# Performance work log

Measured on AMD Instinct MI355X. Metric: run time of the kernel, lower is better.

The kernel has to match this reference:

```python
import jax, jax.numpy as jnp
import numpy as np

NEG_INF = -1e16


def setup_inputs() -> dict:
    key = jax.random.key(0)
    k1, k2, k3 = jax.random.split(key, 3)
    B, N, C, D = 8, 4096, 64, 64
    inputs = jax.random.normal(k1, (B, N, C), dtype=jnp.float32)
    graph = jax.random.randint(k2, (N, N), 0, 2, dtype=jnp.int32)
    # xavier_uniform for Linear weight [D, C]
    limit = float(np.sqrt(6.0 / (C + D)))
    W = jax.random.uniform(k3, (D, C), dtype=jnp.float32, minval=-limit, maxval=limit)
    b = jnp.zeros((D,), dtype=jnp.float32)
    return {"inputs": inputs, "graph": graph, "W": W, "b": b}


def reference(inputs, graph, W, b):
    # h = W(inputs): [B, N, D]
    h = jnp.einsum('bnc,dc->bnd', inputs, W)
    # dense pairwise scores: [B, N, N]
    scores = jnp.einsum('bnd,bmd->bnm', h, h)
    # mask non-edges (graph broadcasts over batch)
    scores = jnp.where(graph[None, :, :] == 0, NEG_INF, scores)
    attention = jax.nn.softmax(scores, axis=2)
    out = jnp.einsum('bnm,bmd->bnd', attention, h) + b
    return out
```

## Files before the change

### kernel.cpp

```cpp
#include <hip/hip_runtime.h>
#include <stdint.h>

typedef _Float16 f16x8 __attribute__((ext_vector_type(8)));
typedef _Float16 f16x4 __attribute__((ext_vector_type(4)));
typedef __fp16 half2_t __attribute__((ext_vector_type(2)));
typedef float f32x4 __attribute__((ext_vector_type(4)));

#define LOG2E 1.44269504088896340736f
#define NEGINF (-1e16f)

constexpr int kN = 4096;
constexpr int kD = 64;
constexpr int kB = 8;

__global__ __launch_bounds__(256) void hproj_kernel(const float* __restrict__ x,
                                                    const float* __restrict__ W,
                                                    _Float16* __restrict__ hout,
                                                    _Float16* __restrict__ hTout)
{
    __shared__ float Wt[64][64];
    __shared__ float xs[64][65];
    __shared__ _Float16 ht[64][68];

    const int tid = threadIdx.x;
    const int r   = tid >> 2;
    const int c0  = (tid & 3) * 16;

    #pragma unroll
    for (int j = 0; j < 16; j += 4) {
        const float4 v = *(const float4*)(W + r * 64 + c0 + j);
        Wt[c0 + j + 0][r] = v.x;
        Wt[c0 + j + 1][r] = v.y;
        Wt[c0 + j + 2][r] = v.z;
        Wt[c0 + j + 3][r] = v.w;
    }
    const long rowbase = (long)blockIdx.x * 64;
    #pragma unroll
    for (int j = 0; j < 16; j += 4) {
        const float4 v = *(const float4*)(x + (rowbase + r) * 64 + c0 + j);
        xs[r][c0 + j + 0] = v.x;
        xs[r][c0 + j + 1] = v.y;
        xs[r][c0 + j + 2] = v.z;
        xs[r][c0 + j + 3] = v.w;
    }
    __syncthreads();

    const int d0 = (tid & 3) * 16;
    f32x4 acc[4] = {{0.f,0.f,0.f,0.f},{0.f,0.f,0.f,0.f},{0.f,0.f,0.f,0.f},{0.f,0.f,0.f,0.f}};
    #pragma unroll 4
    for (int c = 0; c < 64; ++c) {
        const float xv = xs[r][c];
        const f32x4* wrow = (const f32x4*)&Wt[c][d0];
        #pragma unroll
        for (int k = 0; k < 4; ++k) acc[k] += wrow[k] * xv;
    }
    f16x8 o0, o1;
    #pragma unroll
    for (int j = 0; j < 8; ++j) {
        o0[j] = (_Float16)acc[j >> 2][j & 3];
        o1[j] = (_Float16)acc[2 + (j >> 2)][j & 3];
    }
    *(f16x8*)(hout + (rowbase + r) * 64 + d0)     = o0;
    *(f16x8*)(hout + (rowbase + r) * 64 + d0 + 8) = o1;

    #pragma unroll
    for (int j = 0; j < 8; ++j) {
        ht[r][d0 + j]     = o0[j];
        ht[r][d0 + 8 + j] = o1[j];
    }
    __syncthreads();

    const int bb = blockIdx.x >> 6;
    const int n0 = (int)(rowbase & (kN - 1));
    const int dr = tid >> 2;
    const int c4 = (tid & 3) * 16;
    f16x8 t0, t1;
    #pragma unroll
    for (int j = 0; j < 8; ++j) {
        t0[j] = ht[c4 + j][dr];
        t1[j] = ht[c4 + 8 + j][dr];
    }
    _Float16* dst = hTout + (long)bb * kD * kN + (long)dr * kN + n0 + c4;
    *(f16x8*)(dst)     = t0;
    *(f16x8*)(dst + 8) = t1;
}

__global__ __launch_bounds__(256) void bitpack_kernel(const int* __restrict__ g,
                                                      uint32_t* __restrict__ mw)
{
    const long w = (long)blockIdx.x * 256 + threadIdx.x;
    const int4* p = (const int4*)(g + w * 32);
    uint32_t bits = 0;
    #pragma unroll
    for (int j = 0; j < 8; ++j) {
        const int4 v = p[j];
        bits |= (uint32_t)(v.x != 0) << (j * 4 + 0);
        bits |= (uint32_t)(v.y != 0) << (j * 4 + 1);
        bits |= (uint32_t)(v.z != 0) << (j * 4 + 2);
        bits |= (uint32_t)(v.w != 0) << (j * 4 + 3);
    }
    mw[w] = bits;
}

__global__ __launch_bounds__(256) void masktr_kernel(const uint32_t* __restrict__ mw,
                                                     uint64_t* __restrict__ wmout)
{
    const int tid  = threadIdx.x;
    const int wv   = tid >> 6;
    const int lane = tid & 63;
    const int ll   = lane & 15;
    const int lg   = lane >> 4;
    const int pair = blockIdx.x * 4 + wv;
    const int q16  = pair >> 6;
    const int kv64 = pair & 63;

    const uint2 u = *(const uint2*)(mw + (long)(q16 * 16 + ll) * 128 + kv64 * 2);

    uint64_t Wb[16];
    #pragma unroll
    for (int s = 0; s < 16; ++s) {
        const int t = s >> 2, rr = s & 3;
        const uint32_t word = (t >= 2) ? u.y : u.x;
        const int pos = 8 * lg + 4 * (t & 1) + rr;
        Wb[s] = __ballot(((word >> pos) & 1u) != 0);
    }

    const int s = lane;
    uint64_t a0 = (s & 1) ? Wb[1]  : Wb[0];
    uint64_t a1 = (s & 1) ? Wb[3]  : Wb[2];
    uint64_t a2 = (s & 1) ? Wb[5]  : Wb[4];
    uint64_t a3 = (s & 1) ? Wb[7]  : Wb[6];
    uint64_t a4 = (s & 1) ? Wb[9]  : Wb[8];
    uint64_t a5 = (s & 1) ? Wb[11] : Wb[10];
    uint64_t a6 = (s & 1) ? Wb[13] : Wb[12];
    uint64_t a7 = (s & 1) ? Wb[15] : Wb[14];
    uint64_t b0 = (s & 2) ? a1 : a0;
    uint64_t b1 = (s & 2) ? a3 : a2;
    uint64_t b2 = (s & 2) ? a5 : a4;
    uint64_t b3 = (s & 2) ? a7 : a6;
    uint64_t c0 = (s & 4) ? b1 : b0;
    uint64_t c1 = (s & 4) ? b3 : b2;
    uint64_t v  = (s & 8) ? c1 : c0;
    if (lane < 16) wmout[(long)pair * 16 + lane] = v;
}

__global__ __launch_bounds__(512, 4) void attn_kernel(const _Float16* __restrict__ h,
                                                      const _Float16* __restrict__ hT,
                                                      const uint64_t* __restrict__ wmask,
                                                      const float* __restrict__ bias,
                                                      float* __restrict__ outp,
                                                      _Float16* __restrict__ pO,
                                                      float* __restrict__ pml,
                                                      int kvlen)
{
    __shared__ alignas(16) char Kl[2][8192];
    __shared__ alignas(16) char Vt[2][8192];

    const int b     = blockIdx.y;
    const int split = blockIdx.z;
    const int q0    = blockIdx.x * 256;
    const int tid   = threadIdx.x;
    const int wave  = tid >> 6;
    const int lane  = tid & 63;
    const int lg    = lane >> 4;
    const int ll    = lane & 15;

    const _Float16* hb  = h  + (long)b * kN * kD;
    const _Float16* hTb = hT + (long)b * kD * kN;
    const int kv_base = split * kvlen;
    const int NT      = kvlen / 64;

    const int qA = q0 + wave * 32 + ll;
    const int qB = qA + 16;
    const f16x8 qfA0 = *(const f16x8*)(hb + qA * 64 + lg * 8);
    const f16x8 qfA1 = *(const f16x8*)(hb + qA * 64 + 32 + lg * 8);
    const f16x8 qfB0 = *(const f16x8*)(hb + qB * 64 + lg * 8);
    const f16x8 qfB1 = *(const f16x8*)(hb + qB * 64 + 32 + lg * 8);

    f16x8 vone;
    {
        const _Float16 o = (ll == 0) ? (_Float16)1.0f : (_Float16)0.0f;
        #pragma unroll
        for (int j = 0; j < 8; ++j) vone[j] = o;
    }

    f32x4 OaccA[4] = {{0.f,0.f,0.f,0.f},{0.f,0.f,0.f,0.f},{0.f,0.f,0.f,0.f},{0.f,0.f,0.f,0.f}};
    f32x4 OaccB[4] = {{0.f,0.f,0.f,0.f},{0.f,0.f,0.f,0.f},{0.f,0.f,0.f,0.f},{0.f,0.f,0.f,0.f}};
    f32x4 Oacc4A = {0.f, 0.f, 0.f, 0.f};
    f32x4 Oacc4B = {0.f, 0.f, 0.f, 0.f};
    float m_runA = NEGINF, m_runB = NEGINF;
    float mmA = NEGINF * LOG2E, mmB = NEGINF * LOG2E;
    float negv = NEGINF;

    const int sr  = tid >> 3;
    const int sc8 = (tid & 7) * 8;
    const int srp = (sr & 0x23) | ((sr & 0x18) >> 1) | ((sr & 0x4) << 2);

    const int kw = srp * 128 + ((sc8 * 2) ^ ((srp & 7) << 4));
    const int vw = sr  * 128 + ((sc8 * 2) ^ ((sr  & 7) << 4));
    const int rb0 = ll * 128 + (((lg * 16))      ^ ((ll & 7) << 4));
    const int rb1 = ll * 128 + (((64 + lg * 16)) ^ ((ll & 7) << 4));

    char* const KB = (char*)Kl;
    char* const VB = (char*)Vt;

    const _Float16* gK = hb  + (long)(kv_base + sr) * 64 + sc8;
    const _Float16* gV = hTb + (long)sr * kN + kv_base + sc8;

    const int wuni = __builtin_amdgcn_readfirstlane(wave);
    const uint64_t* __restrict__ wmpA =
        wmask + ((long)(blockIdx.x * 16 + wuni * 2) * 64 + (kv_base >> 6)) * 16;
    const uint64_t* __restrict__ wmpB = wmpA + (long)64 * 16;

    {
        const f16x8 a0 = *(const f16x8*)(gK);
        const f16x8 b0 = *(const f16x8*)(gV);
        *(f16x8*)(KB + kw) = a0;
        *(f16x8*)(VB + vw) = b0;
        gK += 64 * 64;  gV += 64;
    }

    union PF { half2_t hh[4]; f16x8 v; };

#define SOFTMAX_FRAG(S_, WM_, OACC_, OACC4_, MRUN_, MM_, PF1_, PF2_)             \
    do {                                                                         \
        _Pragma("unroll")                                                        \
        for (int t = 0; t < 4; ++t) {                                            \
            _Pragma("unroll")                                                    \
            for (int rr = 0; rr < 4; ++rr) {                                     \
                float sv = S_[t][rr];                                            \
                asm("v_cndmask_b32 %0, %1, %2, %3"                               \
                    : "=v"(sv) : "v"(negv), "v"(sv), "s"(WM_[t * 4 + rr]));      \
                S_[t][rr] = sv;                                                  \
            }                                                                    \
        }                                                                        \
        float mx0 = fmaxf(fmaxf(S_[0][0], S_[0][1]), fmaxf(S_[0][2], S_[0][3])); \
        float mx1 = fmaxf(fmaxf(S_[1][0], S_[1][1]), fmaxf(S_[1][2], S_[1][3])); \
        float mx2 = fmaxf(fmaxf(S_[2][0], S_[2][1]), fmaxf(S_[2][2], S_[2][3])); \
        float mx3 = fmaxf(fmaxf(S_[3][0], S_[3][1]), fmaxf(S_[3][2], S_[3][3])); \
        float mloc = fmaxf(fmaxf(mx0, mx1), fmaxf(mx2, mx3));                    \
        mloc = fmaxf(mloc, __shfl_xor(mloc, 16));                                \
        mloc = fmaxf(mloc, __shfl_xor(mloc, 32));                                \
        if (__any(mloc > MRUN_ + 8.f)) {                                         \
            const float mnew = fmaxf(MRUN_, mloc);                               \
            const float scl  = __builtin_amdgcn_exp2f((MRUN_ - mnew) * LOG2E);   \
            MRUN_ = mnew;                                                        \
            MM_   = mnew * LOG2E;                                                \
            _Pragma("unroll")                                                    \
            for (int dt = 0; dt < 4; ++dt) OACC_[dt] *= scl;                     \
            OACC4_ *= scl;                                                       \
        }                                                                        \
        _Pragma("unroll")                                                        \
        for (int t = 0; t < 4; ++t) {                                            \
            _Pragma("unroll")                                                    \
            for (int rr = 0; rr < 4; ++rr)                                       \
                S_[t][rr] = __builtin_amdgcn_exp2f(fmaf(S_[t][rr], LOG2E, -MM_));\
        }                                                                        \
        PF1_.hh[0] = __builtin_amdgcn_cvt_pkrtz(S_[0][0], S_[0][1]);             \
        PF1_.hh[1] = __builtin_amdgcn_cvt_pkrtz(S_[0][2], S_[0][3]);             \
        PF1_.hh[2] = __builtin_amdgcn_cvt_pkrtz(S_[1][0], S_[1][1]);             \
        PF1_.hh[3] = __builtin_amdgcn_cvt_pkrtz(S_[1][2], S_[1][3]);             \
        PF2_.hh[0] = __builtin_amdgcn_cvt_pkrtz(S_[2][0], S_[2][1]);             \
        PF2_.hh[1] = __builtin_amdgcn_cvt_pkrtz(S_[2][2], S_[2][3]);             \
        PF2_.hh[2] = __builtin_amdgcn_cvt_pkrtz(S_[3][0], S_[3][1]);             \
        PF2_.hh[3] = __builtin_amdgcn_cvt_pkrtz(S_[3][2], S_[3][3]);             \
    } while (0)

#define TILE_BODY(IT, CB, NB)                                                    \
    do {                                                                         \
        const int it_ = (IT);                                                    \
                  \
        f16x8 nk0{}, nv0{};                                                      \
        if (it_ + 1 < NT) {                                                      \
            nk0 = *(const f16x8*)(gK);                                           \
            nv0 = *(const f16x8*)(gV);                                           \
            gK += 64 * 64;  gV += 64;                                            \
        }                                                                        \
                         \
        asm volatile("s_waitcnt lgkmcnt(0)" ::: "memory");                       \
        __builtin_amdgcn_s_barrier();                                            \
        __builtin_amdgcn_sched_barrier(0);                                       \
                \
        uint64_t WMA[16], WMB[16];                                               \
        _Pragma("unroll")                                                        \
        for (int s5 = 0; s5 < 16; ++s5) WMA[s5] = wmpA[(long)it_ * 16 + s5];     \
        _Pragma("unroll")                                                        \
        for (int s5 = 0; s5 < 16; ++s5) WMB[s5] = wmpB[(long)it_ * 16 + s5];     \
                                       \
        f32x4 SA[4], SB[4];                                                      \
        __builtin_amdgcn_s_setprio(1);                                           \
        _Pragma("unroll")                                                        \
        for (int t = 0; t < 4; ++t) {                                            \
            const f16x8 k0 = *(const f16x8*)(KB + (CB) + rb0 + t * 2048);        \
            const f16x8 k1 = *(const f16x8*)(KB + (CB) + rb1 + t * 2048);        \
            f32x4 sa = {0.f, 0.f, 0.f, 0.f};                                     \
            f32x4 sb = {0.f, 0.f, 0.f, 0.f};                                     \
            sa = __builtin_amdgcn_mfma_f32_16x16x32_f16(k0, qfA0, sa, 0, 0, 0);  \
            sa = __builtin_amdgcn_mfma_f32_16x16x32_f16(k1, qfA1, sa, 0, 0, 0);  \
            sb = __builtin_amdgcn_mfma_f32_16x16x32_f16(k0, qfB0, sb, 0, 0, 0);  \
            sb = __builtin_amdgcn_mfma_f32_16x16x32_f16(k1, qfB1, sb, 0, 0, 0);  \
            SA[t] = sa;                                                          \
            SB[t] = sb;                                                          \
        }                                                                        \
        __builtin_amdgcn_s_setprio(0);                                           \
                                  \
        if (it_ + 1 < NT) {                                                      \
            *(f16x8*)(KB + (NB) + kw) = nk0;                                     \
            *(f16x8*)(VB + (NB) + vw) = nv0;                                     \
        }                                                                        \
        PF pfA1, pfA2, pfB1, pfB2;                                               \
        SOFTMAX_FRAG(SA, WMA, OaccA, Oacc4A, m_runA, mmA, pfA1, pfA2);           \
        SOFTMAX_FRAG(SB, WMB, OaccB, Oacc4B, m_runB, mmB, pfB1, pfB2);           \
                                       \
        __builtin_amdgcn_s_setprio(1);                                           \
        _Pragma("unroll")                                                        \
        for (int dt = 0; dt < 4; ++dt) {                                         \
            const f16x8 v0 = *(const f16x8*)(VB + (CB) + rb0 + dt * 2048);       \
            const f16x8 v1 = *(const f16x8*)(VB + (CB) + rb1 + dt * 2048);       \
            OaccA[dt] = __builtin_amdgcn_mfma_f32_16x16x32_f16(v0, pfA1.v, OaccA[dt], 0, 0, 0); \
            OaccA[dt] = __builtin_amdgcn_mfma_f32_16x16x32_f16(v1, pfA2.v, OaccA[dt], 0, 0, 0); \
            OaccB[dt] = __builtin_amdgcn_mfma_f32_16x16x32_f16(v0, pfB1.v, OaccB[dt], 0, 0, 0); \
            OaccB[dt] = __builtin_amdgcn_mfma_f32_16x16x32_f16(v1, pfB2.v, OaccB[dt], 0, 0, 0); \
        }                                                                        \
        Oacc4A = __builtin_amdgcn_mfma_f32_16x16x32_f16(vone, pfA1.v, Oacc4A, 0, 0, 0); \
        Oacc4A = __builtin_amdgcn_mfma_f32_16x16x32_f16(vone, pfA2.v, Oacc4A, 0, 0, 0); \
        Oacc4B = __builtin_amdgcn_mfma_f32_16x16x32_f16(vone, pfB1.v, Oacc4B, 0, 0, 0); \
        Oacc4B = __builtin_amdgcn_mfma_f32_16x16x32_f16(vone, pfB2.v, Oacc4B, 0, 0, 0); \
        __builtin_amdgcn_s_setprio(0);                                           \
    } while (0)

    for (int ith = 0; ith < NT; ith += 2) {
        TILE_BODY(ith,     0,    8192);
        TILE_BODY(ith + 1, 8192, 0);
    }
#undef TILE_BODY
#undef SOFTMAX_FRAG

    const float lsumA = __shfl(Oacc4A[0], ll, 64);
    const float lsumB = __shfl(Oacc4B[0], ll, 64);
    const float invA  = (lsumA > 0.f) ? (1.0f / lsumA) : 0.f;
    const float invB  = (lsumB > 0.f) ? (1.0f / lsumB) : 0.f;

    if (outp != nullptr) {
        #pragma unroll
        for (int dt = 0; dt < 4; ++dt) {
            const int dbase = dt * 16 + lg * 4;
            const f32x4 bv = *(const f32x4*)(bias + dbase);
            f32x4 oa, ob;
            #pragma unroll
            for (int rr = 0; rr < 4; ++rr) {
                oa[rr] = OaccA[dt][rr] * invA + bv[rr];
                ob[rr] = OaccB[dt][rr] * invB + bv[rr];
            }
            *(f32x4*)(outp + ((long)b * kN + qA) * 64 + dbase) = oa;
            *(f32x4*)(outp + ((long)b * kN + qB) * 64 + dbase) = ob;
        }
    } else {
        const long srowA = (long)split * kB * kN + (long)b * kN + qA;
        const long srowB = srowA + 16;
        #pragma unroll
        for (int dt = 0; dt < 4; ++dt) {
            const int dbase = dt * 16 + lg * 4;
            f16x4 pa, pb;
            #pragma unroll
            for (int rr = 0; rr < 4; ++rr) {
                pa[rr] = (_Float16)(OaccA[dt][rr] * invA);
                pb[rr] = (_Float16)(OaccB[dt][rr] * invB);
            }
            *(f16x4*)(pO + srowA * 64 + dbase) = pa;
            *(f16x4*)(pO + srowB * 64 + dbase) = pb;
        }
        if (lane < 16) {
            pml[srowA * 2 + 0] = m_runA;
            pml[srowA * 2 + 1] = lsumA;
            pml[srowB * 2 + 0] = m_runB;
            pml[srowB * 2 + 1] = lsumB;
        }
    }
}

__global__ __launch_bounds__(256) void combine_kernel(const _Float16* __restrict__ pO,
                                                      const float* __restrict__ pml,
                                                      const float* __restrict__ bias,
                                                      float* __restrict__ outp,
                                                      int ks)
{
    const long idx = (long)blockIdx.x * 256 + threadIdx.x;
    const long row = idx >> 4;
    const int  d4  = (int)(idx & 15) * 4;

    float M = NEGINF;
    for (int s = 0; s < ks; ++s)
        M = fmaxf(M, pml[((long)s * kB * kN + row) * 2]);

    float L = 0.f;
    f32x4 acc = {0.f, 0.f, 0.f, 0.f};
    for (int s = 0; s < ks; ++s) {
        const long srow = (long)s * kB * kN + row;
        const float m = pml[srow * 2 + 0];
        const float l = pml[srow * 2 + 1];
        const float w = l * __builtin_amdgcn_exp2f((m - M) * LOG2E);
        L += w;
        const f16x4 o = *(const f16x4*)(pO + srow * 64 + d4);
        #pragma unroll
        for (int j = 0; j < 4; ++j) acc[j] += (float)o[j] * w;
    }
    const float invL = (L > 0.f) ? (1.0f / L) : 0.f;
    const f32x4 bv = *(const f32x4*)(bias + d4);
    *(f32x4*)(outp + row * 64 + d4) = acc * invL + bv;
}

extern "C" void kernel_launch(void* const* d_in, const int* in_sizes, int n_in,
                              void* d_out, int out_size, void* d_ws, size_t ws_size,
                              hipStream_t stream) {
    const float*  x     = (const float*)d_in[0];
    const int*    graph = (const int*)d_in[1];
    const float*  W     = (const float*)d_in[2];
    const float*  bias  = (const float*)d_in[3];
    float*        outp  = (float*)d_out;

    char* ws = (char*)d_ws;
    _Float16* hptr  = (_Float16*)ws;
    uint32_t* mwptr = (uint32_t*)(ws + (4u << 20));
    _Float16* hTptr = (_Float16*)(ws + (6u << 20));
    uint64_t* wmptr = (uint64_t*)(ws + (10u << 20));

    int ks = 1;
    if      (ws_size >= ((size_t)30 << 20)) ks = 4;
    else if (ws_size >= ((size_t)21 << 20)) ks = 2;

    _Float16* pO  = (_Float16*)(ws + (12u << 20));
    float*    pml = (float*)(ws + (12u << 20) + (size_t)ks * (4u << 20));

    hproj_kernel<<<dim3(kB * kN / 64), dim3(256), 0, stream>>>(x, W, hptr, hTptr);
    bitpack_kernel<<<dim3(kN * (kN / 32) / 256), dim3(256), 0, stream>>>(graph, mwptr);
    masktr_kernel<<<dim3(256 * 64 / 4), dim3(256), 0, stream>>>(mwptr, wmptr);

    if (ks == 1) {
        attn_kernel<<<dim3(kN / 256, kB, 1), dim3(512), 0, stream>>>(
            hptr, hTptr, wmptr, bias, outp, nullptr, nullptr, kN);
    } else {
        attn_kernel<<<dim3(kN / 256, kB, ks), dim3(512), 0, stream>>>(
            hptr, hTptr, wmptr, bias, nullptr, pO, pml, kN / ks);
        combine_kernel<<<dim3(kB * kN * 16 / 256), dim3(256), 0, stream>>>(
            pO, pml, bias, outp, ks);
    }
}
```

Before: 85.23 us.

## Fuse graph bitpack and mask transpose into one kernel; allow 8-way KV split

Merges the bitpack and mask-transpose kernels, so the new kernel reads the int32 graph directly and builds the ballot masks without an intermediate packed buffer. This removes one launch and a global write/read round trip of the packed mask. It also compacts the workspace layout and adds a ks=8 split-KV option when the workspace is large enough, which means more partial outputs for the combine kernel to merge. Each lane's loads from the graph are now 16-byte strided reads and may coalesce less well than the old bitpack reads.

```diff
diff --git a/kernel.cpp b/kernel.cpp
--- a/kernel.cpp
+++ b/kernel.cpp
@@ -85,25 +85,8 @@
     *(f16x8*)(dst + 8) = t1;
 }
 
-__global__ __launch_bounds__(256) void bitpack_kernel(const int* __restrict__ g,
-                                                      uint32_t* __restrict__ mw)
-{
-    const long w = (long)blockIdx.x * 256 + threadIdx.x;
-    const int4* p = (const int4*)(g + w * 32);
-    uint32_t bits = 0;
-    #pragma unroll
-    for (int j = 0; j < 8; ++j) {
-        const int4 v = p[j];
-        bits |= (uint32_t)(v.x != 0) << (j * 4 + 0);
-        bits |= (uint32_t)(v.y != 0) << (j * 4 + 1);
-        bits |= (uint32_t)(v.z != 0) << (j * 4 + 2);
-        bits |= (uint32_t)(v.w != 0) << (j * 4 + 3);
-    }
-    mw[w] = bits;
-}
-
-__global__ __launch_bounds__(256) void masktr_kernel(const uint32_t* __restrict__ mw,
-                                                     uint64_t* __restrict__ wmout)
+__global__ __launch_bounds__(256) void graphmask_kernel(const int* __restrict__ g,
+                                                        uint64_t* __restrict__ wmout)
 {
     const int tid  = threadIdx.x;
     const int wv   = tid >> 6;
@@ -114,15 +97,24 @@
     const int q16  = pair >> 6;
     const int kv64 = pair & 63;
 
-    const uint2 u = *(const uint2*)(mw + (long)(q16 * 16 + ll) * 128 + kv64 * 2);
+    const int* gr = g + (long)(q16 * 16 + ll) * kN + kv64 * 64 + 8 * lg;
+    const int4 u0 = *(const int4*)(gr);
+    const int4 u1 = *(const int4*)(gr + 4);
+    const int4 u2 = *(const int4*)(gr + 32);
+    const int4 u3 = *(const int4*)(gr + 36);
+
+    int gv[16];
+    gv[0] = u0.x;  gv[1] = u0.y;  gv[2] = u0.z;  gv[3] = u0.w;
+    gv[4] = u1.x;  gv[5] = u1.y;  gv[6] = u1.z;  gv[7] = u1.w;
+    gv[8] = u2.x;  gv[9] = u2.y;  gv[10] = u2.z;  gv[11] = u2.w;
+    gv[12] = u3.x; gv[13] = u3.y; gv[14] = u3.z;  gv[15] = u3.w;
 
     uint64_t Wb[16];
     #pragma unroll
     for (int s = 0; s < 16; ++s) {
         const int t = s >> 2, rr = s & 3;
-        const uint32_t word = (t >= 2) ? u.y : u.x;
-        const int pos = 8 * lg + 4 * (t & 1) + rr;
-        Wb[s] = __ballot(((word >> pos) & 1u) != 0);
+        const int j = (t >= 2 ? 8 : 0) + 4 * (t & 1) + rr;
+        Wb[s] = __ballot(gv[j] != 0);
     }
 
     const int s = lane;
@@ -421,20 +413,19 @@
 
     char* ws = (char*)d_ws;
     _Float16* hptr  = (_Float16*)ws;
-    uint32_t* mwptr = (uint32_t*)(ws + (4u << 20));
-    _Float16* hTptr = (_Float16*)(ws + (6u << 20));
-    uint64_t* wmptr = (uint64_t*)(ws + (10u << 20));
+    _Float16* hTptr = (_Float16*)(ws + (4u << 20));
+    uint64_t* wmptr = (uint64_t*)(ws + (8u << 20));
 
     int ks = 1;
-    if      (ws_size >= ((size_t)30 << 20)) ks = 4;
-    else if (ws_size >= ((size_t)21 << 20)) ks = 2;
-
-    _Float16* pO  = (_Float16*)(ws + (12u << 20));
-    float*    pml = (float*)(ws + (12u << 20) + (size_t)ks * (4u << 20));
+    if      (ws_size >= ((size_t)47 << 20)) ks = 8;
+    else if (ws_size >= ((size_t)28 << 20)) ks = 4;
+    else if (ws_size >= ((size_t)19 << 20)) ks = 2;
+
+    _Float16* pO  = (_Float16*)(ws + (10u << 20));
+    float*    pml = (float*)(ws + (10u << 20) + (size_t)ks * (4u << 20));
 
     hproj_kernel<<<dim3(kB * kN / 64), dim3(256), 0, stream>>>(x, W, hptr, hTptr);
-    bitpack_kernel<<<dim3(kN * (kN / 32) / 256), dim3(256), 0, stream>>>(graph, mwptr);
-    masktr_kernel<<<dim3(256 * 64 / 4), dim3(256), 0, stream>>>(mwptr, wmptr);
+    graphmask_kernel<<<dim3(256 * 64 / 4), dim3(256), 0, stream>>>(graph, wmptr);
 
     if (ks == 1) {
         attn_kernel<<<dim3(kN / 256, kB, 1), dim3(512), 0, stream>>>(
```

Result: slower. 87.88 us (+3.1%).
